# Kernel tuning notes

Measured on AMD Instinct MI355X. Metric: run time of the kernel, lower is better.

The kernel has to match this reference:

```python
import jax, jax.numpy as jnp
import numpy as np

N_NODES = 100000


def _gcn_layer(x, W, b, src, dst, inv_sqrt_deg):
    # transform first (cheaper when out_dim <= in_dim), then normalized aggregate
    h = x @ W  # [N, out]
    coeff = (inv_sqrt_deg[src] * inv_sqrt_deg[dst])[:, None]  # [E,1] sym norm
    msgs = h[src] * coeff  # [E, out]
    agg = jax.ops.segment_sum(msgs, dst, num_segments=N_NODES)  # [N, out]
    return agg + b


def setup_inputs() -> dict:
    key = jax.random.key(0)
    ks = jax.random.split(key, 8)
    n, e = N_NODES, 1600000
    x = jax.random.normal(ks[0], (n, 256), dtype=jnp.float32)
    src = jax.random.randint(ks[1], (e,), 0, n)
    dst = jax.random.randint(ks[2], (e,), 0, n)
    W1 = jax.random.normal(ks[3], (256, 128), dtype=jnp.float32) * 0.05
    b1 = jax.random.normal(ks[4], (128,), dtype=jnp.float32) * 0.05
    W2 = jax.random.normal(ks[5], (128, 40), dtype=jnp.float32) * 0.05
    b2 = jax.random.normal(ks[6], (40,), dtype=jnp.float32) * 0.05
    return {"x": x, "src": src, "dst": dst, "W1": W1, "b1": b1, "W2": W2, "b2": b2}


def reference(x, src, dst, W1, b1, W2, b2):
    # degree-based symmetric normalization D^{-1/2} A D^{-1/2}
    ones = jnp.ones(src.shape, dtype=x.dtype)
    deg = jax.ops.segment_sum(ones, dst, num_segments=N_NODES)
    inv_sqrt_deg = jnp.where(deg > 0, jax.lax.rsqrt(jnp.maximum(deg, 1.0)), 0.0)
    h = _gcn_layer(x, W1, b1, src, dst, inv_sqrt_deg)
    h = jax.nn.relu(h)
    h = _gcn_layer(h, W2, b2, src, dst, inv_sqrt_deg)
    return h
```

## Files before the change

kernel.cpp:

```cpp
#include <hip/hip_runtime.h>
#include <hip/hip_bf16.h>


#define CHUNK   4096
#define NPB     512
#define NBUCK   196
#define BBCAP   9216

typedef __bf16 bf16x8 __attribute__((ext_vector_type(8)));
typedef float floatx4 __attribute__((ext_vector_type(4)));

__device__ inline unsigned short f2bf(float f) {
    unsigned u = __float_as_uint(f);
    u += 0x7FFF + ((u >> 16) & 1);
    return (unsigned short)(u >> 16);
}
__device__ inline float bflo(unsigned p) { return __uint_as_float(p << 16); }
__device__ inline float bfhi(unsigned p) { return __uint_as_float(p & 0xFFFF0000u); }

__global__ __launch_bounds__(256) void k_part(const int* __restrict__ src,
                                              const int* __restrict__ dst,
                                              int* __restrict__ gcursor,
                                              unsigned* __restrict__ buckets, int E) {
    __shared__ unsigned srec[CHUNK];
    __shared__ unsigned char sb8[CHUNK];
    __shared__ int hist[NBUCK];
    __shared__ int lbase[NBUCK];
    __shared__ int gbase[NBUCK];
    __shared__ int scanbuf[256];
    int t = threadIdx.x;
    int base = blockIdx.x * CHUNK;
    int cnt = min(CHUNK, E - base);
    for (int i = t; i < NBUCK; i += 256) hist[i] = 0;
    __syncthreads();

    unsigned rec[16];
    unsigned br[16];
    bool valid[4];
    #pragma unroll
    for (int k = 0; k < 4; ++k) {
        int e0 = k * 1024 + t * 4;
        valid[k] = (e0 < cnt);
        if (valid[k]) {
            int4 s4 = *(const int4*)&src[base + e0];
            int4 d4 = *(const int4*)&dst[base + e0];
            int ss[4] = {s4.x, s4.y, s4.z, s4.w};
            int dd[4] = {d4.x, d4.y, d4.z, d4.w};
            #pragma unroll
            for (int j = 0; j < 4; ++j) {
                int b = dd[j] >> 9;
                int r = atomicAdd(&hist[b], 1);
                rec[k * 4 + j] = (unsigned)ss[j] | ((unsigned)(dd[j] & 511) << 17);
                br[k * 4 + j] = (unsigned)b | ((unsigned)r << 8);
            }
        }
    }
    __syncthreads();
    scanbuf[t] = (t < NBUCK) ? hist[t] : 0;
    __syncthreads();
    for (int s = 1; s < 256; s <<= 1) {
        int v = (t >= s) ? scanbuf[t - s] : 0;
        __syncthreads();
        scanbuf[t] += v;
        __syncthreads();
    }
    if (t < NBUCK) {
        lbase[t] = scanbuf[t] - hist[t];
        gbase[t] = atomicAdd(&gcursor[t], hist[t]);
    }
    __syncthreads();
    #pragma unroll
    for (int k = 0; k < 4; ++k) {
        if (valid[k]) {
            #pragma unroll
            for (int j = 0; j < 4; ++j) {
                unsigned b = br[k * 4 + j] & 255u;
                unsigned r = br[k * 4 + j] >> 8;
                int p = lbase[b] + (int)r;
                srec[p] = rec[k * 4 + j];
                sb8[p] = (unsigned char)b;
            }
        }
    }
    __syncthreads();
    for (int i = t; i < cnt; i += 256) {
        int b = sb8[i];
        int pos = gbase[b] + (i - lbase[b]);
        if (pos < BBCAP) buckets[(size_t)b * BBCAP + pos] = srec[i];
    }
}

__global__ __launch_bounds__(256) void k_count(const unsigned* __restrict__ buckets,
                                               const int* __restrict__ gcursor,
                                               int* __restrict__ deg, int N) {
    __shared__ int hist[NPB];
    int b = blockIdx.x;
    for (int i = threadIdx.x; i < NPB; i += 256) hist[i] = 0;
    __syncthreads();
    int cnt = min(gcursor[b], BBCAP);
    const unsigned* bk = &buckets[(size_t)b * BBCAP];
    for (int i = threadIdx.x; i < cnt; i += 256)
        atomicAdd(&hist[bk[i] >> 17], 1);
    __syncthreads();
    int node0 = b << 9;
    for (int i = threadIdx.x; i < NPB; i += 256)
        if (node0 + i < N) deg[node0 + i] = hist[i];
}

__global__ void k_isd_offsets(const int* __restrict__ deg, float* __restrict__ isd,
                              int* __restrict__ offsets, int* __restrict__ counter, int N) {
    int n = blockIdx.x * blockDim.x + threadIdx.x;
    int lane = threadIdx.x & 63;
    int d = (n < N) ? deg[n] : 0;
    if (n <= N) isd[n] = (d > 0) ? rsqrtf((float)d) : 0.f;
    int dp = (d + 15) & ~15;
    int pref = dp;
    #pragma unroll
    for (int sh = 1; sh < 64; sh <<= 1) {
        int t = __shfl_up(pref, sh);
        if (lane >= sh) pref += t;
    }
    int total = __shfl(pref, 63);
    int base = 0;
    if (lane == 63) base = atomicAdd(counter, total);
    base = __shfl(base, 63);
    if (n < N) offsets[n] = base + pref - dp;
}

__global__ __launch_bounds__(256) void k_place(const unsigned* __restrict__ buckets,
                                               const int* __restrict__ gcursor,
                                               const int* __restrict__ offsets,
                                               const int* __restrict__ deg,
                                               int* __restrict__ csr, int N) {
    __shared__ int cur[NPB];
    int b = blockIdx.x;
    int node0 = b << 9;
    for (int i = threadIdx.x; i < NPB; i += 256)
        cur[i] = (node0 + i < N) ? offsets[node0 + i] : 0;
    __syncthreads();
    int cnt = min(gcursor[b], BBCAP);
    const unsigned* bk = &buckets[(size_t)b * BBCAP];
    for (int i = threadIdx.x; i < cnt; i += 256) {
        unsigned r = bk[i];
        int p = atomicAdd(&cur[r >> 17], 1);
        csr[p] = (int)(r & 0x1FFFFu);
    }
    __syncthreads();
    for (int i = threadIdx.x; i < NPB; i += 256) {
        int n = node0 + i;
        if (n < N) {
            int d = deg[n];
            int st = offsets[n] + d;
            int en = offsets[n] + ((d + 15) & ~15);
            for (int p = st; p < en; ++p) csr[p] = N;
        }
    }
}

__global__ void k_prep_w1(const float* __restrict__ W1, unsigned short* __restrict__ w1s,
                          unsigned* __restrict__ h2z) {
    if (blockIdx.x == 0 && threadIdx.x < 36) h2z[threadIdx.x] = 0;
    int flat = blockIdx.x * 256 + threadIdx.x;
    int kt = flat >> 9;
    int nt = (flat >> 6) & 7;
    int lane = flat & 63;
    int kbase = kt * 32 + ((lane >> 4) << 3);
    int n = nt * 16 + (lane & 15);
    unsigned short v[8];
    #pragma unroll
    for (int j = 0; j < 8; ++j) v[j] = f2bf(W1[(size_t)(kbase + j) * 128 + n]);
    unsigned short* d = &w1s[(size_t)flat * 8];
    *(short4*)(d)     = make_short4(v[0], v[1], v[2], v[3]);
    *(short4*)(d + 4) = make_short4(v[4], v[5], v[6], v[7]);
}

__global__ __launch_bounds__(256) void k_gemm1(const float* __restrict__ X,
                                               const unsigned short* __restrict__ w1s,
                                               const float* __restrict__ isd,
                                               unsigned short* __restrict__ H, int N) {
    __shared__ __align__(16) unsigned short smem[8192];
    unsigned short* sA = smem;
    unsigned short* sB = smem + 2048;
    int tid = threadIdx.x;
    int lane = tid & 63;
    int wave = tid >> 6;
    int wr = wave >> 1;
    int wc = wave & 1;
    int m0 = blockIdx.x * 64;

    floatx4 acc[2][4] = {};

    for (int kt = 0; kt < 8; ++kt) {
        #pragma unroll
        for (int i = 0; i < 2; ++i) {
            int f = tid * 2 + i;
            int row = f >> 3;
            int c4 = (f & 7) * 4;
            float4 v = make_float4(0.f, 0.f, 0.f, 0.f);
            int grow = m0 + row;
            if (grow < N) v = *(const float4*)&X[(size_t)grow * 256 + kt * 32 + c4];
            int mt = row >> 4;
            int flane = (row & 15) | ((c4 >> 3) << 4);
            int j0 = c4 & 7;
            unsigned short* d = &sA[(size_t)(mt * 64 + flane) * 8 + j0];
            *(short4*)d = make_short4(f2bf(v.x), f2bf(v.y), f2bf(v.z), f2bf(v.w));
        }
        {
            const float4* srcp = (const float4*)&w1s[(size_t)kt * 4096];
            float4* dstp = (float4*)sB;
            dstp[tid] = srcp[tid];
            dstp[tid + 256] = srcp[tid + 256];
        }
        __syncthreads();
        bf16x8 a[2], b[4];
        #pragma unroll
        for (int p = 0; p < 2; ++p)
            a[p] = *(const bf16x8*)&sA[(size_t)((wr * 2 + p) * 64 + lane) * 8];
        #pragma unroll
        for (int q = 0; q < 4; ++q)
            b[q] = *(const bf16x8*)&sB[(size_t)((wc * 4 + q) * 64 + lane) * 8];
        #pragma unroll
        for (int p = 0; p < 2; ++p)
            #pragma unroll
            for (int q = 0; q < 4; ++q)
                acc[p][q] = __builtin_amdgcn_mfma_f32_16x16x32_bf16(a[p], b[q], acc[p][q], 0, 0, 0);
        __syncthreads();
    }
    float sc[2][4];
    #pragma unroll
    for (int p = 0; p < 2; ++p)
        #pragma unroll
        for (int r = 0; r < 4; ++r) {
            int g = m0 + wr * 32 + p * 16 + ((lane >> 4) << 2) + r;
            sc[p][r] = isd[g > N ? N : g];
        }
    #pragma unroll
    for (int p = 0; p < 2; ++p)
        #pragma unroll
        for (int q = 0; q < 4; ++q)
            #pragma unroll
            for (int r = 0; r < 4; ++r) {
                int rl = wr * 32 + p * 16 + ((lane >> 4) << 2) + r;
                int c = wc * 64 + q * 16 + (lane & 15);
                smem[rl * 128 + c] = f2bf(acc[p][q][r] * sc[p][r]);
            }
    __syncthreads();
    #pragma unroll
    for (int i = 0; i < 4; ++i) {
        int f = tid + i * 256;
        int row = f >> 4;
        int c8 = (f & 15) * 8;
        int grow = m0 + row;
        if (grow <= N)
            *(float4*)&H[(size_t)grow * 128 + c8] = *(const float4*)&smem[row * 128 + c8];
    }
}

__global__ __launch_bounds__(256) void k_agg1(const unsigned* __restrict__ Hu,
                                              const int* __restrict__ csr,
                                              const float* __restrict__ isd,
                                              const int* __restrict__ offsets,
                                              const int* __restrict__ deg,
                                              const float* __restrict__ b1,
                                              unsigned* __restrict__ H1u, int N) {
    int w = __builtin_amdgcn_readfirstlane((blockIdx.x * blockDim.x + threadIdx.x) >> 6);
    int lane = threadIdx.x & 63;
    int n0 = w * 4;
    if (n0 >= N) return;
    int startk[4], nbk[4];
    float acc0[4] = {0.f, 0.f, 0.f, 0.f};
    float acc1[4] = {0.f, 0.f, 0.f, 0.f};
    int maxnb = 0;
    #pragma unroll
    for (int k = 0; k < 4; ++k) {
        int n = n0 + k;
        bool v = (n < N);
        startk[k] = v ? offsets[n] : 0;
        nbk[k] = v ? (deg[n] + 15) >> 4 : 0;
        maxnb = max(maxnb, nbk[k]);
    }
    for (int ib = 0; ib < maxnb; ++ib) {
        unsigned p[4][16];
        #pragma unroll
        for (int k = 0; k < 4; ++k) {
            if (ib < nbk[k]) {
                int b0 = startk[k] + ib * 16;
                int s[16];
                #pragma unroll
                for (int j = 0; j < 16; ++j) s[j] = csr[b0 + j];
                #pragma unroll
                for (int j = 0; j < 16; ++j) p[k][j] = Hu[(size_t)s[j] * 64 + lane];
            }
        }
        #pragma unroll
        for (int k = 0; k < 4; ++k) {
            if (ib < nbk[k]) {
                #pragma unroll
                for (int j = 0; j < 16; ++j) {
                    acc0[k] += bflo(p[k][j]);
                    acc1[k] += bfhi(p[k][j]);
                }
            }
        }
    }
    float bl = b1[2 * lane];
    float bh = b1[2 * lane + 1];
    #pragma unroll
    for (int k = 0; k < 4; ++k) {
        int n = n0 + k;
        if (n < N) {
            float isdn = isd[n];
            float r0 = fmaxf(fmaf(isdn, acc0[k], bl), 0.f);
            float r1 = fmaxf(fmaf(isdn, acc1[k], bh), 0.f);
            H1u[(size_t)n * 64 + lane] = (unsigned)f2bf(r0) | ((unsigned)f2bf(r1) << 16);
        }
    }
}

__global__ __launch_bounds__(256) void k_gemm2(const unsigned short* __restrict__ H1,
                                               const float* __restrict__ W2,
                                               const float* __restrict__ isd,
                                               unsigned short* __restrict__ H2, int N) {
    __shared__ float sH[64][132];
    __shared__ float sW[128 * 40];
    int tid = threadIdx.x;
    int block_row = blockIdx.x * 64;
    for (int i = tid; i < 64 * 16; i += 256) {
        int r = i >> 4;
        int c8 = (i & 15) * 8;
        int grow = block_row + r;
        uint4 v = make_uint4(0, 0, 0, 0);
        if (grow < N) v = *(const uint4*)&H1[(size_t)grow * 128 + c8];
        float* d = &sH[r][c8];
        d[0] = bflo(v.x); d[1] = bfhi(v.x);
        d[2] = bflo(v.y); d[3] = bfhi(v.y);
        d[4] = bflo(v.z); d[5] = bfhi(v.z);
        d[6] = bflo(v.w); d[7] = bfhi(v.w);
    }
    for (int i = tid; i < 1280; i += 256)
        *(float4*)&sW[i * 4] = *(const float4*)&W2[(size_t)i * 4];
    __syncthreads();

    int row = tid >> 2;
    int c0 = (tid & 3) * 10;
    float acc[10] = {};
    for (int k = 0; k < 128; ++k) {
        float hv = sH[row][k];
        #pragma unroll
        for (int j = 0; j < 5; ++j) {
            float2 wv = *(const float2*)&sW[k * 40 + c0 + 2 * j];
            acc[2 * j]     = fmaf(hv, wv.x, acc[2 * j]);
            acc[2 * j + 1] = fmaf(hv, wv.y, acc[2 * j + 1]);
        }
    }
    int grow = block_row + row;
    if (grow < N) {
        float scn = isd[grow];
        unsigned* o = (unsigned*)&H2[(size_t)grow * 40 + c0];
        #pragma unroll
        for (int j = 0; j < 5; ++j)
            o[j] = (unsigned)f2bf(acc[2 * j] * scn) |
                   ((unsigned)f2bf(acc[2 * j + 1] * scn) << 16);
    }
}

__global__ __launch_bounds__(256) void k_agg2(const unsigned* __restrict__ Hu2,
                                              const int* __restrict__ csr,
                                              const float* __restrict__ isd,
                                              const int* __restrict__ offsets,
                                              const int* __restrict__ deg,
                                              const float* __restrict__ b2,
                                              float* __restrict__ out, int N) {
    int w = __builtin_amdgcn_readfirstlane((blockIdx.x * blockDim.x + threadIdx.x) >> 6);
    int lane = threadIdx.x & 63;
    int n0 = w * 4;
    if (n0 >= N) return;
    int sub = lane >> 5;
    int c = lane & 31;
    int startk[4], nbk[4];
    float acc0[4] = {0.f, 0.f, 0.f, 0.f};
    float acc1[4] = {0.f, 0.f, 0.f, 0.f};
    int maxnb = 0;
    #pragma unroll
    for (int k = 0; k < 4; ++k) {
        int n = n0 + k;
        bool v = (n < N);
        startk[k] = v ? offsets[n] : 0;
        nbk[k] = v ? (deg[n] + 15) >> 4 : 0;
        maxnb = max(maxnb, nbk[k]);
    }
    for (int ib = 0; ib < maxnb; ++ib) {
        unsigned q[4][8];
        #pragma unroll
        for (int k = 0; k < 4; ++k) {
            if (ib < nbk[k]) {
                int b0 = startk[k] + ib * 16;
                int s[8];
                #pragma unroll
                for (int j = 0; j < 8; ++j) s[j] = csr[b0 + (j << 1) + sub];
                #pragma unroll
                for (int j = 0; j < 8; ++j) q[k][j] = Hu2[(size_t)s[j] * 20 + c];
            }
        }
        #pragma unroll
        for (int k = 0; k < 4; ++k) {
            if (ib < nbk[k]) {
                #pragma unroll
                for (int j = 0; j < 8; ++j) {
                    acc0[k] += bflo(q[k][j]);
                    acc1[k] += bfhi(q[k][j]);
                }
            }
        }
    }
    #pragma unroll
    for (int k = 0; k < 4; ++k) {
        acc0[k] += __shfl(acc0[k], lane + 32);
        acc1[k] += __shfl(acc1[k], lane + 32);
    }
    if (lane < 20) {
        #pragma unroll
        for (int k = 0; k < 4; ++k) {
            int n = n0 + k;
            if (n < N) {
                float isdn = isd[n];
                *(float2*)&out[(size_t)n * 40 + 2 * lane] =
                    make_float2(fmaf(isdn, acc0[k], b2[2 * lane]),
                                fmaf(isdn, acc1[k], b2[2 * lane + 1]));
            }
        }
    }
}

extern "C" void kernel_launch(void* const* d_in, const int* in_sizes, int n_in,
                              void* d_out, int out_size, void* d_ws, size_t ws_size,
                              hipStream_t stream) {
    const float* x  = (const float*)d_in[0];
    const int*  src = (const int*)d_in[1];
    const int*  dst = (const int*)d_in[2];
    const float* W1 = (const float*)d_in[3];
    const float* b1 = (const float*)d_in[4];
    const float* W2 = (const float*)d_in[5];
    const float* b2 = (const float*)d_in[6];
    float* out = (float*)d_out;

    const int N = in_sizes[0] / 256;
    const int E = in_sizes[1];

    char* w = (char*)d_ws;
    auto alloc = [&](size_t bytes) -> void* {
        void* p = (void*)w;
        w += (bytes + 15) & ~(size_t)15;
        return p;
    };
    int*      gcursor = (int*)alloc(256 * 4);
    int*      counter = (int*)alloc(16);
    int*      deg     = (int*)alloc((size_t)N * 4);
    float*    isd     = (float*)alloc((size_t)(N + 1) * 4);
    int*      offsets = (int*)alloc((size_t)(N + 1) * 4);
    unsigned* buckets = (unsigned*)alloc((size_t)NBUCK * BBCAP * 4);
    int*      csr     = (int*)alloc((size_t)(E + 16 * (size_t)N) * 4);
    unsigned short* w1s = (unsigned short*)alloc(32768 * 2);
    unsigned short* h   = (unsigned short*)alloc((size_t)(N + 1) * 128 * 2);
    unsigned short* h1  = (unsigned short*)alloc((size_t)N * 128 * 2);
    unsigned short* h2  = (unsigned short*)alloc(((size_t)(N + 1) * 20 + 16) * 4);

    hipMemsetAsync(gcursor, 0, 256 * 4 + 16, stream);

    int nchunk = (E + CHUNK - 1) / CHUNK;
    k_part<<<nchunk, 256, 0, stream>>>(src, dst, gcursor, buckets, E);
    k_count<<<NBUCK, 256, 0, stream>>>(buckets, gcursor, deg, N);
    k_isd_offsets<<<(N + 256) / 256, 256, 0, stream>>>(deg, isd, offsets, counter, N);
    k_place<<<NBUCK, 256, 0, stream>>>(buckets, gcursor, offsets, deg, csr, N);
    k_prep_w1<<<16, 256, 0, stream>>>(W1, w1s, (unsigned*)h2 + (size_t)N * 20);
    k_gemm1<<<(N + 63) / 64, 256, 0, stream>>>(x, w1s, isd, h, N);
    k_agg1<<<(N + 15) / 16, 256, 0, stream>>>((const unsigned*)h, csr, isd, offsets, deg,
                                              b1, (unsigned*)h1, N);
    k_gemm2<<<(N + 63) / 64, 256, 0, stream>>>(h1, W2, isd, h2, N);
    k_agg2<<<(N + 15) / 16, 256, 0, stream>>>((const unsigned*)h2, csr, isd, offsets, deg,
                                              b2, out, N);
}
```

Measured before the change: 408.2 us.

## Split feature tables into column halves pinned to XCD groups for gather locality

Intermediate feature tables H and H2 are stored as two column-half planes instead of one row-major array. The aggregation kernels remap block indices so blocks on XCDs 0-3 gather only from the first half and blocks on XCDs 4-7 only from the second. The intent is to shrink each XCD's random-gather working set so it fits its L2/cache better. In exchange, each node's neighbor list is read twice, agg2 leaves some lanes idle (c>=10), and the mapping assumes round-robin block-to-XCD dispatch.

After: 443.4 us. 8.6% more time.

```diff
diff --git a/kernel.cpp b/kernel.cpp
--- a/kernel.cpp
+++ b/kernel.cpp
@@ -158,8 +158,13 @@
 }
 
 __global__ void k_prep_w1(const float* __restrict__ W1, unsigned short* __restrict__ w1s,
-                          unsigned* __restrict__ h2z) {
-    if (blockIdx.x == 0 && threadIdx.x < 36) h2z[threadIdx.x] = 0;
+                          unsigned* __restrict__ h2p, int N) {
+    if (blockIdx.x == 0 && threadIdx.x < 32) {
+        size_t H2S = (size_t)(N + 1) * 10 + 16;
+        int hh = threadIdx.x >> 4;
+        int i = threadIdx.x & 15;
+        h2p[(size_t)hh * H2S + (size_t)N * 10 + i] = 0;
+    }
     int flat = blockIdx.x * 256 + threadIdx.x;
     int kt = flat >> 9;
     int nt = (flat >> 6) & 7;
@@ -177,7 +182,7 @@
 __global__ __launch_bounds__(256) void k_gemm1(const float* __restrict__ X,
                                                const unsigned short* __restrict__ w1s,
                                                const float* __restrict__ isd,
-                                               unsigned short* __restrict__ H, int N) {
+                                               unsigned* __restrict__ Hp, int N) {
     __shared__ __align__(16) unsigned short smem[8192];
     unsigned short* sA = smem;
     unsigned short* sB = smem + 2048;
@@ -187,6 +192,7 @@
     int wr = wave >> 1;
     int wc = wave & 1;
     int m0 = blockIdx.x * 64;
+    size_t HS = (size_t)(N + 1) * 32;
 
     floatx4 acc[2][4] = {};
 
@@ -251,28 +257,40 @@
         int row = f >> 4;
         int c8 = (f & 15) * 8;
         int grow = m0 + row;
-        if (grow <= N)
-            *(float4*)&H[(size_t)grow * 128 + c8] = *(const float4*)&smem[row * 128 + c8];
-    }
-}
-
-__global__ __launch_bounds__(256) void k_agg1(const unsigned* __restrict__ Hu,
+        if (grow <= N) {
+            int cu = c8 >> 1;
+            int half = cu >> 5;
+            int cin = cu & 31;
+            *(float4*)&Hp[(size_t)half * HS + (size_t)grow * 32 + cin] =
+                *(const float4*)&smem[row * 128 + c8];
+        }
+    }
+}
+
+__global__ __launch_bounds__(256) void k_agg1(const unsigned* __restrict__ Hp,
                                               const int* __restrict__ csr,
                                               const float* __restrict__ isd,
                                               const int* __restrict__ offsets,
                                               const int* __restrict__ deg,
                                               const float* __restrict__ b1,
                                               unsigned* __restrict__ H1u, int N) {
-    int w = __builtin_amdgcn_readfirstlane((blockIdx.x * blockDim.x + threadIdx.x) >> 6);
+    int b = blockIdx.x;
+    int xcd = b & 7;
+    int half = xcd >> 2;
+    int hb = (b >> 3) * 4 + (xcd & 3);
+    int wave = threadIdx.x >> 6;
     int lane = threadIdx.x & 63;
-    int n0 = w * 4;
+    int n0 = __builtin_amdgcn_readfirstlane(hb * 8 + wave * 2);
     if (n0 >= N) return;
-    int startk[4], nbk[4];
-    float acc0[4] = {0.f, 0.f, 0.f, 0.f};
-    float acc1[4] = {0.f, 0.f, 0.f, 0.f};
+    size_t HS = (size_t)(N + 1) * 32;
+    const unsigned* P = Hp + (size_t)half * HS;
+    int sub = lane >> 5;
+    int c = lane & 31;
+    int startk[2], nbk[2];
+    float a0[2] = {0.f, 0.f}, a1[2] = {0.f, 0.f};
     int maxnb = 0;
     #pragma unroll
-    for (int k = 0; k < 4; ++k) {
+    for (int k = 0; k < 2; ++k) {
         int n = n0 + k;
         bool v = (n < N);
         startk[k] = v ? offsets[n] : 0;
@@ -280,39 +298,48 @@
         maxnb = max(maxnb, nbk[k]);
     }
     for (int ib = 0; ib < maxnb; ++ib) {
-        unsigned p[4][16];
-        #pragma unroll
-        for (int k = 0; k < 4; ++k) {
+        unsigned p[2][8];
+        #pragma unroll
+        for (int k = 0; k < 2; ++k) {
             if (ib < nbk[k]) {
                 int b0 = startk[k] + ib * 16;
-                int s[16];
+                int s[8];
                 #pragma unroll
-                for (int j = 0; j < 16; ++j) s[j] = csr[b0 + j];
+                for (int j = 0; j < 8; ++j) s[j] = csr[b0 + (j << 1) + sub];
                 #pragma unroll
-                for (int j = 0; j < 16; ++j) p[k][j] = Hu[(size_t)s[j] * 64 + lane];
-            }
-        }
-        #pragma unroll
-        for (int k = 0; k < 4; ++k) {
+                for (int j = 0; j < 8; ++j) p[k][j] = P[(size_t)s[j] * 32 + c];
+            }
+        }
+        #pragma unroll
+        for (int k = 0; k < 2; ++k) {
             if (ib < nbk[k]) {
                 #pragma unroll
-                for (int j = 0; j < 16; ++j) {
-                    acc0[k] += bflo(p[k][j]);
-                    acc1[k] += bfhi(p[k][j]);
+                for (int j = 0; j < 8; ++j) {
+                    a0[k] += bflo(p[k][j]);
+                    a1[k] += bfhi(p[k][j]);
                 }
             }
         }
     }
-    float bl = b1[2 * lane];
-    float bh = b1[2 * lane + 1];
-    #pragma unroll
-    for (int k = 0; k < 4; ++k) {
-        int n = n0 + k;
-        if (n < N) {
-            float isdn = isd[n];
-            float r0 = fmaxf(fmaf(isdn, acc0[k], bl), 0.f);
-            float r1 = fmaxf(fmaf(isdn, acc1[k], bh), 0.f);
-            H1u[(size_t)n * 64 + lane] = (unsigned)f2bf(r0) | ((unsigned)f2bf(r1) << 16);
+    #pragma unroll
+    for (int k = 0; k < 2; ++k) {
+        a0[k] += __shfl(a0[k], lane + 32);
+        a1[k] += __shfl(a1[k], lane + 32);
+    }
+    if (lane < 32) {
+        int col0 = 2 * (half * 32 + lane);
+        float bl = b1[col0];
+        float bh = b1[col0 + 1];
+        #pragma unroll
+        for (int k = 0; k < 2; ++k) {
+            int n = n0 + k;
+            if (n < N) {
+                float isdn = isd[n];
+                float r0 = fmaxf(fmaf(isdn, a0[k], bl), 0.f);
+                float r1 = fmaxf(fmaf(isdn, a1[k], bh), 0.f);
+                H1u[(size_t)n * 64 + half * 32 + lane] =
+                    (unsigned)f2bf(r0) | ((unsigned)f2bf(r1) << 16);
+            }
         }
     }
 }
@@ -320,11 +347,12 @@
 __global__ __launch_bounds__(256) void k_gemm2(const unsigned short* __restrict__ H1,
                                                const float* __restrict__ W2,
                                                const float* __restrict__ isd,
-                                               unsigned short* __restrict__ H2, int N) {
+                                               unsigned* __restrict__ H2p, int N) {
     __shared__ float sH[64][132];
     __shared__ float sW[128 * 40];
     int tid = threadIdx.x;
     int block_row = blockIdx.x * 64;
+    size_t H2S = (size_t)(N + 1) * 10 + 16;
     for (int i = tid; i < 64 * 16; i += 256) {
         int r = i >> 4;
         int c8 = (i & 15) * 8;
@@ -356,7 +384,9 @@
     int grow = block_row + row;
     if (grow < N) {
         float scn = isd[grow];
-        unsigned* o = (unsigned*)&H2[(size_t)grow * 40 + c0];
+        int half = c0 >= 20;
+        int c0h = c0 - half * 20;
+        unsigned* o = &H2p[(size_t)half * H2S + (size_t)grow * 10 + (c0h >> 1)];
         #pragma unroll
         for (int j = 0; j < 5; ++j)
             o[j] = (unsigned)f2bf(acc[2 * j] * scn) |
@@ -364,22 +394,28 @@
     }
 }
 
-__global__ __launch_bounds__(256) void k_agg2(const unsigned* __restrict__ Hu2,
+__global__ __launch_bounds__(256) void k_agg2(const unsigned* __restrict__ H2p,
                                               const int* __restrict__ csr,
                                               const float* __restrict__ isd,
                                               const int* __restrict__ offsets,
                                               const int* __restrict__ deg,
                                               const float* __restrict__ b2,
                                               float* __restrict__ out, int N) {
-    int w = __builtin_amdgcn_readfirstlane((blockIdx.x * blockDim.x + threadIdx.x) >> 6);
+    int b = blockIdx.x;
+    int xcd = b & 7;
+    int half = xcd >> 2;
+    int hb = (b >> 3) * 4 + (xcd & 3);
+    int wave = threadIdx.x >> 6;
     int lane = threadIdx.x & 63;
-    int n0 = w * 4;
+    int n0 = __builtin_amdgcn_readfirstlane(hb * 16 + wave * 4);
     if (n0 >= N) return;
-    int sub = lane >> 5;
-    int c = lane & 31;
+    size_t H2S = (size_t)(N + 1) * 10 + 16;
+    const unsigned* P = H2p + (size_t)half * H2S;
+    int sub = lane >> 4;
+    int c = lane & 15;
     int startk[4], nbk[4];
-    float acc0[4] = {0.f, 0.f, 0.f, 0.f};
-    float acc1[4] = {0.f, 0.f, 0.f, 0.f};
+    float a0[4] = {0.f, 0.f, 0.f, 0.f};
+    float a1[4] = {0.f, 0.f, 0.f, 0.f};
     int maxnb = 0;
     #pragma unroll
     for (int k = 0; k < 4; ++k) {
@@ -390,43 +426,48 @@
         maxnb = max(maxnb, nbk[k]);
     }
     for (int ib = 0; ib < maxnb; ++ib) {
-        unsigned q[4][8];
+        unsigned q[4][4];
         #pragma unroll
         for (int k = 0; k < 4; ++k) {
             if (ib < nbk[k]) {
                 int b0 = startk[k] + ib * 16;
-                int s[8];
+                int s[4];
                 #pragma unroll
-                for (int j = 0; j < 8; ++j) s[j] = csr[b0 + (j << 1) + sub];
+                for (int j = 0; j < 4; ++j) s[j] = csr[b0 + (j << 2) + sub];
                 #pragma unroll
-                for (int j = 0; j < 8; ++j) q[k][j] = Hu2[(size_t)s[j] * 20 + c];
+                for (int j = 0; j < 4; ++j)
+                    q[k][j] = (c < 10) ? P[(size_t)s[j] * 10 + c] : 0u;
             }
         }
         #pragma unroll
         for (int k = 0; k < 4; ++k) {
             if (ib < nbk[k]) {
                 #pragma unroll
-                for (int j = 0; j < 8; ++j) {
-                    acc0[k] += bflo(q[k][j]);
-                    acc1[k] += bfhi(q[k][j]);
+                for (int j = 0; j < 4; ++j) {
+                    a0[k] += bflo(q[k][j]);
+                    a1[k] += bfhi(q[k][j]);
                 }
             }
         }
     }
     #pragma unroll
     for (int k = 0; k < 4; ++k) {
-        acc0[k] += __shfl(acc0[k], lane + 32);
-        acc1[k] += __shfl(acc1[k], lane + 32);
-    }
-    if (lane < 20) {
+        a0[k] += __shfl(a0[k], lane + 32);
+        a1[k] += __shfl(a1[k], lane + 32);
+        a0[k] += __shfl(a0[k], lane + 16);
+        a1[k] += __shfl(a1[k], lane + 16);
+    }
+    if (lane < 10) {
+        int col0 = half * 20 + 2 * lane;
+        float bl = b2[col0];
+        float bh = b2[col0 + 1];
         #pragma unroll
         for (int k = 0; k < 4; ++k) {
             int n = n0 + k;
             if (n < N) {
                 float isdn = isd[n];
-                *(float2*)&out[(size_t)n * 40 + 2 * lane] =
-                    make_float2(fmaf(isdn, acc0[k], b2[2 * lane]),
-                                fmaf(isdn, acc1[k], b2[2 * lane + 1]));
+                *(float2*)&out[(size_t)n * 40 + col0] =
+                    make_float2(fmaf(isdn, a0[k], bl), fmaf(isdn, a1[k], bh));
             }
         }
     }
@@ -453,6 +494,8 @@
         w += (bytes + 15) & ~(size_t)15;
         return p;
     };
+    size_t HS  = (size_t)(N + 1) * 32;
+    size_t H2S = (size_t)(N + 1) * 10 + 16;
     int*      gcursor = (int*)alloc(256 * 4);
     int*      counter = (int*)alloc(16);
     int*      deg     = (int*)alloc((size_t)N * 4);
@@ -461,9 +504,9 @@
     unsigned* buckets = (unsigned*)alloc((size_t)NBUCK * BBCAP * 4);
     int*      csr     = (int*)alloc((size_t)(E + 16 * (size_t)N) * 4);
     unsigned short* w1s = (unsigned short*)alloc(32768 * 2);
-    unsigned short* h   = (unsigned short*)alloc((size_t)(N + 1) * 128 * 2);
-    unsigned short* h1  = (unsigned short*)alloc((size_t)N * 128 * 2);
-    unsigned short* h2  = (unsigned short*)alloc(((size_t)(N + 1) * 20 + 16) * 4);
+    unsigned* h  = (unsigned*)alloc(2 * HS * 4);
+    unsigned short* h1 = (unsigned short*)alloc((size_t)N * 128 * 2);
+    unsigned* h2 = (unsigned*)alloc(2 * H2S * 4);
 
     hipMemsetAsync(gcursor, 0, 256 * 4 + 16, stream);
 
@@ -472,11 +515,11 @@
     k_count<<<NBUCK, 256, 0, stream>>>(buckets, gcursor, deg, N);
     k_isd_offsets<<<(N + 256) / 256, 256, 0, stream>>>(deg, isd, offsets, counter, N);
     k_place<<<NBUCK, 256, 0, stream>>>(buckets, gcursor, offsets, deg, csr, N);
-    k_prep_w1<<<16, 256, 0, stream>>>(W1, w1s, (unsigned*)h2 + (size_t)N * 20);
+    k_prep_w1<<<16, 256, 0, stream>>>(W1, w1s, h2, N);
     k_gemm1<<<(N + 63) / 64, 256, 0, stream>>>(x, w1s, isd, h, N);
-    k_agg1<<<(N + 15) / 16, 256, 0, stream>>>((const unsigned*)h, csr, isd, offsets, deg,
-                                              b1, (unsigned*)h1, N);
+    int hb1 = (((N + 7) / 8) + 3) & ~3;
+    k_agg1<<<2 * hb1, 256, 0, stream>>>(h, csr, isd, offsets, deg, b1, (unsigned*)h1, N);
     k_gemm2<<<(N + 63) / 64, 256, 0, stream>>>(h1, W2, isd, h2, N);
-    k_agg2<<<(N + 15) / 16, 256, 0, stream>>>((const unsigned*)h2, csr, isd, offsets, deg,
-                                              b2, out, N);
-}
+    int hb2 = (((N + 15) / 16) + 3) & ~3;
+    k_agg2<<<2 * hb2, 256, 0, stream>>>(h2, csr, isd, offsets, deg, b2, out, N);
+}
```
